# Kernel tuning notes

Measured on AMD Instinct MI355X. Metric: run time of the kernel, lower is better.

## Reference

```python
import jax, jax.numpy as jnp
import numpy as np

HIDDEN = 2048
NUM_HEADS = 32
NUM_GROUPS = 8
HEAD_DIM = HIDDEN // NUM_HEADS          # 64
GROUP_DIM = HEAD_DIM * NUM_GROUPS       # 512
HPG = NUM_HEADS // NUM_GROUPS           # heads per group = 4
B, S = 2, 2048


def setup_inputs() -> dict:
    key = jax.random.key(0)
    ks = jax.random.split(key, 6)
    sd = 1.0 / np.sqrt(HIDDEN)
    return {
        "x": jax.random.normal(ks[0], (B, S, HIDDEN), jnp.float32),
        "mask": jnp.ones((1, 1, S, S), jnp.int32),
        "Wq": jax.random.normal(ks[1], (HIDDEN, HIDDEN), jnp.float32) * sd,
        "bq": jnp.zeros((HIDDEN,), jnp.float32),
        "Wk": jax.random.normal(ks[2], (HIDDEN, GROUP_DIM), jnp.float32) * sd,
        "bk": jnp.zeros((GROUP_DIM,), jnp.float32),
        "Wv": jax.random.normal(ks[3], (HIDDEN, GROUP_DIM), jnp.float32) * sd,
        "bv": jnp.zeros((GROUP_DIM,), jnp.float32),
        "Wo": jax.random.normal(ks[4], (HIDDEN, HIDDEN), jnp.float32) * sd,
        "bo": jnp.zeros((HIDDEN,), jnp.float32),
    }


def reference(x, mask, Wq, bq, Wk, bk, Wv, bv, Wo, bo):
    b, s, _ = x.shape
    # projections
    q = x @ Wq + bq                                        # [B,S,H*d]
    k = x @ Wk + bk                                        # [B,S,G*d]
    v = x @ Wv + bv
    # split heads: q heads are group-major (g, p) to match the torch view
    q = q.reshape(b, s, NUM_GROUPS, HPG, HEAD_DIM)         # [B,S,G,P,d]
    k = k.reshape(b, s, NUM_GROUPS, HEAD_DIM)              # [B,S,G,d]
    v = v.reshape(b, s, NUM_GROUPS, HEAD_DIM)
    scale = 1.0 / np.sqrt(HEAD_DIM).astype(np.float32)
    # grouped attention without materializing repeated K/V
    scores = jnp.einsum('bsgpd,btgd->bgpst', q, k) * scale  # [B,G,P,S,T]
    if mask is not None:
        m = mask[:, :, None]                                # [1,1,1,S,T]
        scores = jnp.where(m == 0, jnp.float32(-1e9), scores)
    weights = jax.nn.softmax(scores, axis=-1)
    out = jnp.einsum('bgpst,btgd->bsgpd', weights, v)       # [B,S,G,P,d]
    out = out.reshape(b, s, HIDDEN)
    return out @ Wo + bo
```

## Files before the change

### kernel.cpp

```cpp
#include <hip/hip_runtime.h>
#include <hip/hip_bf16.h>


#define DEVINL __device__ __forceinline__

typedef __attribute__((ext_vector_type(8))) short bf16x8;
typedef __attribute__((ext_vector_type(4))) float f32x4;

DEVINL unsigned short f2bf(float f) {
  unsigned u = __builtin_bit_cast(unsigned, f);
  u += 0x7fffu + ((u >> 16) & 1u);
  return (unsigned short)(u >> 16);
}

DEVINL unsigned pk2bf(float a, float b) {
  __hip_bfloat162 h = __float22bfloat162_rn(float2{a, b});
  unsigned r;
  __builtin_memcpy(&r, &h, 4);
  return r;
}

DEVINL void gl_lds16(const void* g, void* l) {
  __builtin_amdgcn_global_load_lds(
      (const __attribute__((address_space(1))) void*)g,
      (__attribute__((address_space(3))) void*)l, 16, 0, 0);
}

__global__ __launch_bounds__(256)
void prep_k(const float* __restrict__ x,
            const float* __restrict__ Wq, const float* __restrict__ Wk,
            const float* __restrict__ Wv, const float* __restrict__ Wo,
            const int* __restrict__ mask,
            unsigned short* __restrict__ xb,
            unsigned short* __restrict__ WqT, unsigned short* __restrict__ WkT,
            unsigned short* __restrict__ WvT, unsigned short* __restrict__ WoT,
            int* __restrict__ flags)
{
  __shared__ float tile[64][68];
  __shared__ int fl[4];
  int blk = blockIdx.x;
  const int tid = threadIdx.x;
  if (blk < 4096) {
    size_t base = (size_t)blk * 2048 + tid * 8;
    float4 f0 = *(const float4*)&x[base];
    float4 f1 = *(const float4*)&x[base + 4];
    uint4 o;
    o.x = pk2bf(f0.x, f0.y); o.y = pk2bf(f0.z, f0.w);
    o.z = pk2bf(f1.x, f1.y); o.w = pk2bf(f1.z, f1.w);
    *(uint4*)&xb[base] = o;
    return;
  }
  blk -= 4096;
  if (blk >= 2560) {
    int fb = blk - 2560;
    int qt = fb >> 5, tt = fb & 31;
    bool hz = false;
#pragma unroll
    for (int it = 0; it < 8; ++it) {
      int l = it * 1024 + tid * 4;
      int row = l >> 6, col = l & 63;
      int4 mv = *(const int4*)&mask[(size_t)(qt * 128 + row) * 2048 + tt * 64 + col];
      hz |= (mv.x == 0) | (mv.y == 0) | (mv.z == 0) | (mv.w == 0);
    }
    unsigned long long bal = __ballot(hz);
    if ((tid & 63) == 0) fl[tid >> 6] = (bal != 0ull) ? 1 : 0;
    __syncthreads();
    if (tid == 0) flags[fb] = fl[0] | fl[1] | fl[2] | fl[3];
    return;
  }
  const float* W; unsigned short* WT; int N;
  if (blk < 1024)      { W = Wq; WT = WqT; N = 2048; }
  else if (blk < 1280) { W = Wk; WT = WkT; N = 512;  blk -= 1024; }
  else if (blk < 1536) { W = Wv; WT = WvT; N = 512;  blk -= 1280; }
  else                 { W = Wo; WT = WoT; N = 2048; blk -= 1536; }
  const int kt = blk & 31, nt = blk >> 5;
  const int k0 = kt * 64, n0 = nt * 64;
  const int tr = tid >> 4, tc4 = (tid & 15) * 4;
#pragma unroll
  for (int it = 0; it < 4; ++it) {
    int k = it * 16 + tr;
    float4 v = *(const float4*)&W[(size_t)(k0 + k) * N + n0 + tc4];
    tile[tc4 + 0][k] = v.x; tile[tc4 + 1][k] = v.y;
    tile[tc4 + 2][k] = v.z; tile[tc4 + 3][k] = v.w;
  }
  __syncthreads();
#pragma unroll
  for (int it = 0; it < 4; ++it) {
    int n = it * 16 + tr;
    uint2 o;
    o.x = pk2bf(tile[n][tc4 + 0], tile[n][tc4 + 1]);
    o.y = pk2bf(tile[n][tc4 + 2], tile[n][tc4 + 3]);
    *(uint2*)&WT[(size_t)(n0 + n) * 2048 + k0 + tc4] = o;
  }
}

__global__ __launch_bounds__(256)
void mm_qkv(const unsigned short* __restrict__ A,
            const unsigned short* __restrict__ Wt,
            const float* __restrict__ bq, const float* __restrict__ bk,
            const float* __restrict__ bv,
            unsigned short* __restrict__ qb, unsigned short* __restrict__ kb,
            unsigned short* __restrict__ vb)
{
  __shared__ __align__(16) unsigned short As[128 * 32];
  __shared__ __align__(16) unsigned short Bs[128 * 32];
  const int tid = threadIdx.x;
  const int lane = tid & 63, w = tid >> 6;
  const int l15 = lane & 15, quad = lane >> 4;
  const int wm = w & 1, wn = w >> 1;
  const int row0 = blockIdx.y * 128;
  const int col0 = blockIdx.x * 128;

  f32x4 acc[4][4];
#pragma unroll
  for (int mt = 0; mt < 4; ++mt)
#pragma unroll
    for (int nt = 0; nt < 4; ++nt) acc[mt][nt] = (f32x4){0.f, 0.f, 0.f, 0.f};

  const int c0 = tid, c1 = 256 + tid;
  const size_t aoff0 = (size_t)(row0 + (c0 >> 2)) * 2048 + (c0 & 3) * 8;
  const size_t aoff1 = (size_t)(row0 + (c1 >> 2)) * 2048 + (c1 & 3) * 8;
  const size_t boff0 = (size_t)(col0 + (c0 >> 2)) * 2048 + (c0 & 3) * 8;
  const size_t boff1 = (size_t)(col0 + (c1 >> 2)) * 2048 + (c1 & 3) * 8;

  for (int k0 = 0; k0 < 2048; k0 += 32) {
    gl_lds16(A + aoff0 + k0, As + (size_t)c0 * 8);
    gl_lds16(A + aoff1 + k0, As + (size_t)c1 * 8);
    gl_lds16(Wt + boff0 + k0, Bs + (size_t)c0 * 8);
    gl_lds16(Wt + boff1 + k0, Bs + (size_t)c1 * 8);
    __syncthreads();
    bf16x8 af[4], bfr[4];
#pragma unroll
    for (int mt = 0; mt < 4; ++mt)
      af[mt] = *(const bf16x8*)&As[(wm * 64 + mt * 16 + l15) * 32 + quad * 8];
#pragma unroll
    for (int nt = 0; nt < 4; ++nt)
      bfr[nt] = *(const bf16x8*)&Bs[(wn * 64 + nt * 16 + l15) * 32 + quad * 8];
#pragma unroll
    for (int mt = 0; mt < 4; ++mt)
#pragma unroll
      for (int nt = 0; nt < 4; ++nt)
        acc[mt][nt] = __builtin_amdgcn_mfma_f32_16x16x32_bf16(
            af[mt], bfr[nt], acc[mt][nt], 0, 0, 0);
    __syncthreads();
  }

  const int rbase = row0 + wm * 64 + quad * 4;
#pragma unroll
  for (int nt = 0; nt < 4; ++nt) {
    const int cg = col0 + wn * 64 + nt * 16 + l15;
#pragma unroll
    for (int mt = 0; mt < 4; ++mt) {
#pragma unroll
      for (int reg = 0; reg < 4; ++reg) {
        const int r = rbase + mt * 16 + reg;
        const int bb = r >> 11, ss = r & 2047;
        float v = acc[mt][nt][reg];
        if (col0 < 2048) {
          v += bq[cg];
          int g = cg >> 8, p = (cg >> 6) & 3, d = cg & 63;
          qb[(((size_t)((bb * 8 + g) * 4 + p)) * 2048 + ss) * 64 + d] =
              f2bf(v * 0.1803368801111244f);
        } else if (col0 < 2560) {
          int cl = cg - 2048;
          v += bk[cl];
          int g = cl >> 6, d = cl & 63;
          kb[((size_t)(bb * 8 + g) * 2048 + ss) * 64 + d] = f2bf(v);
        } else {
          int cl = cg - 2560;
          v += bv[cl];
          int g = cl >> 6, d = cl & 63;
          vb[((size_t)(bb * 8 + g) * 64 + d) * 2048 + ss] = f2bf(v);
        }
      }
    }
  }
}

__global__ __launch_bounds__(256)
void mm_out(const unsigned short* __restrict__ A,
            const unsigned short* __restrict__ Bt,
            const float* __restrict__ bias, float* __restrict__ Of)
{
  __shared__ __align__(16) unsigned short As[128 * 32];
  __shared__ __align__(16) unsigned short Bs[128 * 32];
  const int tid = threadIdx.x;
  const int lane = tid & 63, w = tid >> 6;
  const int l15 = lane & 15, quad = lane >> 4;
  const int wm = w & 1, wn = w >> 1;
  const int row0 = blockIdx.y * 128;
  const int col0 = blockIdx.x * 128;

  f32x4 acc[4][4];
#pragma unroll
  for (int mt = 0; mt < 4; ++mt)
#pragma unroll
    for (int nt = 0; nt < 4; ++nt) acc[mt][nt] = (f32x4){0.f, 0.f, 0.f, 0.f};

  const int c0 = tid, c1 = 256 + tid;
  const size_t aoff0 = (size_t)(row0 + (c0 >> 2)) * 2048 + (c0 & 3) * 8;
  const size_t aoff1 = (size_t)(row0 + (c1 >> 2)) * 2048 + (c1 & 3) * 8;
  const size_t boff0 = (size_t)(col0 + (c0 >> 2)) * 2048 + (c0 & 3) * 8;
  const size_t boff1 = (size_t)(col0 + (c1 >> 2)) * 2048 + (c1 & 3) * 8;

  for (int k0 = 0; k0 < 2048; k0 += 32) {
    gl_lds16(A + aoff0 + k0, As + (size_t)c0 * 8);
    gl_lds16(A + aoff1 + k0, As + (size_t)c1 * 8);
    gl_lds16(Bt + boff0 + k0, Bs + (size_t)c0 * 8);
    gl_lds16(Bt + boff1 + k0, Bs + (size_t)c1 * 8);
    __syncthreads();
    bf16x8 af[4], bfr[4];
#pragma unroll
    for (int mt = 0; mt < 4; ++mt)
      af[mt] = *(const bf16x8*)&As[(wm * 64 + mt * 16 + l15) * 32 + quad * 8];
#pragma unroll
    for (int nt = 0; nt < 4; ++nt)
      bfr[nt] = *(const bf16x8*)&Bs[(wn * 64 + nt * 16 + l15) * 32 + quad * 8];
#pragma unroll
    for (int mt = 0; mt < 4; ++mt)
#pragma unroll
      for (int nt = 0; nt < 4; ++nt)
        acc[mt][nt] = __builtin_amdgcn_mfma_f32_16x16x32_bf16(
            af[mt], bfr[nt], acc[mt][nt], 0, 0, 0);
    __syncthreads();
  }

  const int rbase = row0 + wm * 64 + quad * 4;
#pragma unroll
  for (int nt = 0; nt < 4; ++nt) {
    const int cg = col0 + wn * 64 + nt * 16 + l15;
    const float bvv = bias[cg];
#pragma unroll
    for (int mt = 0; mt < 4; ++mt)
#pragma unroll
      for (int reg = 0; reg < 4; ++reg) {
        const int r = rbase + mt * 16 + reg;
        Of[(size_t)r * 2048 + cg] = acc[mt][nt][reg] + bvv;
      }
  }
}

__global__ __launch_bounds__(256)
void attn_k(const unsigned short* __restrict__ qb,
            const unsigned short* __restrict__ kb,
            const unsigned short* __restrict__ vb,
            const int* __restrict__ mask, const int* __restrict__ flags,
            unsigned short* __restrict__ attnb)
{
  __shared__ __align__(16) unsigned short Ks[64 * 64];
  __shared__ __align__(16) unsigned short Vs[64 * 64];
  __shared__ __align__(16) unsigned short Ps[128 * 72];
  const int tid = threadIdx.x;
  const int lane = tid & 63, w = tid >> 6;
  const int l15 = lane & 15, quad = lane >> 4;
  const int q0 = blockIdx.x * 128;
  const int pr = blockIdx.y;
  const int b = pr >> 4, g = (pr >> 1) & 7, pp = pr & 1;
  const int bg = b * 8 + g;
  const int h0 = g * 4 + pp * 2;

  const unsigned short* Kg = kb + (size_t)bg * 2048 * 64;
  const unsigned short* Vg = vb + (size_t)bg * 64 * 2048;

  bf16x8 qf[2][2][2];
#pragma unroll
  for (int h = 0; h < 2; ++h) {
    const unsigned short* Qg = qb + (size_t)((bg * 4 + pp * 2 + h)) * 2048 * 64;
#pragma unroll
    for (int u = 0; u < 2; ++u) {
      const size_t qrow = (size_t)(q0 + w * 32 + u * 16 + l15) * 64;
      qf[h][u][0] = *(const bf16x8*)&Qg[qrow + quad * 8];
      qf[h][u][1] = *(const bf16x8*)&Qg[qrow + 32 + quad * 8];
    }
  }

  bf16x8 ones;
#pragma unroll
  for (int i = 0; i < 8; ++i) ones[i] = (short)0x3F80;

  f32x4 acc_o[2][4][2];
  f32x4 acc_l[2][2];
#pragma unroll
  for (int h = 0; h < 2; ++h) {
#pragma unroll
    for (int u = 0; u < 2; ++u) acc_l[h][u] = (f32x4){0.f, 0.f, 0.f, 0.f};
#pragma unroll
    for (int dt = 0; dt < 4; ++dt)
#pragma unroll
      for (int u = 0; u < 2; ++u) acc_o[h][dt][u] = (f32x4){0.f, 0.f, 0.f, 0.f};
  }

  const int c0 = tid, c1 = 256 + tid;
  const int kr0 = c0 >> 3, kx0 = ((c0 & 7) ^ (kr0 & 7)) * 8;
  const int kr1 = c1 >> 3, kx1 = ((c1 & 7) ^ (kr1 & 7)) * 8;

  for (int t0 = 0; t0 < 2048; t0 += 64) {
    __syncthreads();
    gl_lds16(Kg + (size_t)(t0 + kr0) * 64 + kx0, Ks + (size_t)c0 * 8);
    gl_lds16(Kg + (size_t)(t0 + kr1) * 64 + kx1, Ks + (size_t)c1 * 8);
    gl_lds16(Vg + (size_t)kr0 * 2048 + t0 + kx0, Vs + (size_t)c0 * 8);
    gl_lds16(Vg + (size_t)kr1 * 2048 + t0 + kx1, Vs + (size_t)c1 * 8);
    __syncthreads();

    bf16x8 kf[4][2];
#pragma unroll
    for (int nt = 0; nt < 4; ++nt) {
      const int trow = nt * 16 + l15, ks = trow & 7;
      kf[nt][0] = *(const bf16x8*)&Ks[trow * 64 + ((quad ^ ks) * 8)];
      kf[nt][1] = *(const bf16x8*)&Ks[trow * 64 + (((4 + quad) ^ ks) * 8)];
    }
    const bool msk = flags[blockIdx.x * 32 + (t0 >> 6)] != 0;

#pragma unroll
    for (int h = 0; h < 2; ++h) {
#pragma unroll
      for (int u = 0; u < 2; ++u) {
        f32x4 st[4];
#pragma unroll
        for (int nt = 0; nt < 4; ++nt) {
          f32x4 z = (f32x4){0.f, 0.f, 0.f, 0.f};
          z = __builtin_amdgcn_mfma_f32_16x16x32_bf16(kf[nt][0], qf[h][u][0], z, 0, 0, 0);
          st[nt] = __builtin_amdgcn_mfma_f32_16x16x32_bf16(kf[nt][1], qf[h][u][1], z, 0, 0, 0);
        }
        if (msk) {
          const size_t mrow = (size_t)(q0 + w * 32 + u * 16 + l15) * 2048;
#pragma unroll
          for (int nt = 0; nt < 4; ++nt) {
            int4 mv = *(const int4*)&mask[mrow + t0 + nt * 16 + quad * 4];
            if (mv.x == 0) st[nt][0] = -1e30f;
            if (mv.y == 0) st[nt][1] = -1e30f;
            if (mv.z == 0) st[nt][2] = -1e30f;
            if (mv.w == 0) st[nt][3] = -1e30f;
          }
        }
        const int srow = w * 32 + u * 16 + l15;
#pragma unroll
        for (int nt = 0; nt < 4; ++nt) {
          float p0 = __builtin_amdgcn_exp2f(st[nt][0]);
          float p1 = __builtin_amdgcn_exp2f(st[nt][1]);
          float p2 = __builtin_amdgcn_exp2f(st[nt][2]);
          float p3 = __builtin_amdgcn_exp2f(st[nt][3]);
          uint2 pkd;
          pkd.x = pk2bf(p0, p1);
          pkd.y = pk2bf(p2, p3);
          *(uint2*)&Ps[srow * 72 + nt * 16 + quad * 4] = pkd;
        }
      }
      asm volatile("s_waitcnt lgkmcnt(0)" ::: "memory");

      bf16x8 pf[2][2];
#pragma unroll
      for (int u = 0; u < 2; ++u) {
        const int srow = w * 32 + u * 16 + l15;
        pf[u][0] = *(const bf16x8*)&Ps[srow * 72 + quad * 8];
        pf[u][1] = *(const bf16x8*)&Ps[srow * 72 + 32 + quad * 8];
        acc_l[h][u] = __builtin_amdgcn_mfma_f32_16x16x32_bf16(ones, pf[u][0], acc_l[h][u], 0, 0, 0);
        acc_l[h][u] = __builtin_amdgcn_mfma_f32_16x16x32_bf16(ones, pf[u][1], acc_l[h][u], 0, 0, 0);
      }
#pragma unroll
      for (int dt = 0; dt < 4; ++dt) {
        const int drow = dt * 16 + l15, ks = drow & 7;
        bf16x8 v0 = *(const bf16x8*)&Vs[drow * 64 + ((quad ^ ks) * 8)];
        bf16x8 v1 = *(const bf16x8*)&Vs[drow * 64 + (((4 + quad) ^ ks) * 8)];
#pragma unroll
        for (int u = 0; u < 2; ++u) {
          acc_o[h][dt][u] = __builtin_amdgcn_mfma_f32_16x16x32_bf16(v0, pf[u][0], acc_o[h][dt][u], 0, 0, 0);
          acc_o[h][dt][u] = __builtin_amdgcn_mfma_f32_16x16x32_bf16(v1, pf[u][1], acc_o[h][dt][u], 0, 0, 0);
        }
      }
    }
  }

#pragma unroll
  for (int h = 0; h < 2; ++h) {
    const int hh = h0 + h;
#pragma unroll
    for (int u = 0; u < 2; ++u) {
      const float inv = 1.0f / acc_l[h][u][0];
      const int s = q0 + w * 32 + u * 16 + l15;
#pragma unroll
      for (int dt = 0; dt < 4; ++dt) {
        uint2 o;
        o.x = pk2bf(acc_o[h][dt][u][0] * inv, acc_o[h][dt][u][1] * inv);
        o.y = pk2bf(acc_o[h][dt][u][2] * inv, acc_o[h][dt][u][3] * inv);
        *(uint2*)&attnb[((size_t)(b * 2048 + s)) * 2048 + hh * 64 + dt * 16 + quad * 4] = o;
      }
    }
  }
}

extern "C" void kernel_launch(void* const* d_in, const int* in_sizes, int n_in,
                              void* d_out, int out_size, void* d_ws, size_t ws_size,
                              hipStream_t stream)
{
  (void)in_sizes; (void)n_in; (void)out_size; (void)ws_size;
  const float* x  = (const float*)d_in[0];
  const int* mask = (const int*)d_in[1];
  const float* Wq = (const float*)d_in[2];
  const float* bq = (const float*)d_in[3];
  const float* Wk = (const float*)d_in[4];
  const float* bk = (const float*)d_in[5];
  const float* Wv = (const float*)d_in[6];
  const float* bv = (const float*)d_in[7];
  const float* Wo = (const float*)d_in[8];
  const float* bo = (const float*)d_in[9];
  float* out = (float*)d_out;

  unsigned short* xb  = (unsigned short*)d_ws;
  unsigned short* WqT = xb  + 8388608;
  unsigned short* WkT = WqT + 4194304;
  unsigned short* WvT = WkT + 1048576;
  unsigned short* WoT = WvT + 1048576;
  unsigned short* qb  = WoT + 4194304;
  unsigned short* kb  = qb  + 8388608;
  unsigned short* vb  = kb  + 2097152;
  int* flags = (int*)(vb + 2097152);
  unsigned short* attnb = xb;

  dim3 blk(256);
  hipLaunchKernelGGL(prep_k, dim3(7168), blk, 0, stream,
                     x, Wq, Wk, Wv, Wo, mask, xb, WqT, WkT, WvT, WoT, flags);
  hipLaunchKernelGGL(mm_qkv, dim3(24, 32), blk, 0, stream,
                     xb, WqT, bq, bk, bv, qb, kb, vb);
  hipLaunchKernelGGL(attn_k, dim3(16, 32), blk, 0, stream,
                     qb, kb, vb, mask, flags, attnb);
  hipLaunchKernelGGL(mm_out, dim3(16, 32), blk, 0, stream,
                     attnb, WoT, bo, out);
}
```

Measured before the change: 354.3 us.

## Deepen GEMM K-tile with swizzled LDS and halve attention query tile

Both GEMM kernels now load 64-wide K tiles into XOR-swizzled LDS, with two MFMA half-steps per barrier pair. This halves the number of syncthreads per K and avoids LDS bank conflicts on fragment reads. The attention kernel drops from 128 to 64 query rows per block, doubling the grid, and uses a per-head P buffer with launch_bounds(256,4) for higher occupancy. The cost is more redundant K/V tile loads across attention blocks and more LDS per GEMM block.

```diff
diff --git a/kernel.cpp b/kernel.cpp
--- a/kernel.cpp
+++ b/kernel.cpp
@@ -102,14 +102,15 @@
             unsigned short* __restrict__ qb, unsigned short* __restrict__ kb,
             unsigned short* __restrict__ vb)
 {
-  __shared__ __align__(16) unsigned short As[128 * 32];
-  __shared__ __align__(16) unsigned short Bs[128 * 32];
+  __shared__ __align__(16) unsigned short As[128 * 64];
+  __shared__ __align__(16) unsigned short Bs[128 * 64];
   const int tid = threadIdx.x;
   const int lane = tid & 63, w = tid >> 6;
   const int l15 = lane & 15, quad = lane >> 4;
   const int wm = w & 1, wn = w >> 1;
   const int row0 = blockIdx.y * 128;
   const int col0 = blockIdx.x * 128;
+  const int sk = l15 & 7;
 
   f32x4 acc[4][4];
 #pragma unroll
@@ -117,31 +118,41 @@
 #pragma unroll
     for (int nt = 0; nt < 4; ++nt) acc[mt][nt] = (f32x4){0.f, 0.f, 0.f, 0.f};
 
-  const int c0 = tid, c1 = 256 + tid;
-  const size_t aoff0 = (size_t)(row0 + (c0 >> 2)) * 2048 + (c0 & 3) * 8;
-  const size_t aoff1 = (size_t)(row0 + (c1 >> 2)) * 2048 + (c1 & 3) * 8;
-  const size_t boff0 = (size_t)(col0 + (c0 >> 2)) * 2048 + (c0 & 3) * 8;
-  const size_t boff1 = (size_t)(col0 + (c1 >> 2)) * 2048 + (c1 & 3) * 8;
-
-  for (int k0 = 0; k0 < 2048; k0 += 32) {
-    gl_lds16(A + aoff0 + k0, As + (size_t)c0 * 8);
-    gl_lds16(A + aoff1 + k0, As + (size_t)c1 * 8);
-    gl_lds16(Wt + boff0 + k0, Bs + (size_t)c0 * 8);
-    gl_lds16(Wt + boff1 + k0, Bs + (size_t)c1 * 8);
-    __syncthreads();
-    bf16x8 af[4], bfr[4];
-#pragma unroll
-    for (int mt = 0; mt < 4; ++mt)
-      af[mt] = *(const bf16x8*)&As[(wm * 64 + mt * 16 + l15) * 32 + quad * 8];
-#pragma unroll
-    for (int nt = 0; nt < 4; ++nt)
-      bfr[nt] = *(const bf16x8*)&Bs[(wn * 64 + nt * 16 + l15) * 32 + quad * 8];
-#pragma unroll
-    for (int mt = 0; mt < 4; ++mt)
+  size_t aoff[4], boff[4];
+#pragma unroll
+  for (int i = 0; i < 4; ++i) {
+    const int c = tid + i * 256;
+    const int r = c >> 3, kx = ((c & 7) ^ (r & 7)) * 8;
+    aoff[i] = (size_t)(row0 + r) * 2048 + kx;
+    boff[i] = (size_t)(col0 + r) * 2048 + kx;
+  }
+
+  for (int k0 = 0; k0 < 2048; k0 += 64) {
+#pragma unroll
+    for (int i = 0; i < 4; ++i)
+      gl_lds16(A + aoff[i] + k0, As + (size_t)(tid + i * 256) * 8);
+#pragma unroll
+    for (int i = 0; i < 4; ++i)
+      gl_lds16(Wt + boff[i] + k0, Bs + (size_t)(tid + i * 256) * 8);
+    __syncthreads();
+#pragma unroll
+    for (int half = 0; half < 2; ++half) {
+      bf16x8 af[4], bfr[4];
+#pragma unroll
+      for (int mt = 0; mt < 4; ++mt)
+        af[mt] = *(const bf16x8*)&As[(wm * 64 + mt * 16 + l15) * 64 +
+                                     (((half * 4 + quad) ^ sk) * 8)];
 #pragma unroll
       for (int nt = 0; nt < 4; ++nt)
-        acc[mt][nt] = __builtin_amdgcn_mfma_f32_16x16x32_bf16(
-            af[mt], bfr[nt], acc[mt][nt], 0, 0, 0);
+        bfr[nt] = *(const bf16x8*)&Bs[(wn * 64 + nt * 16 + l15) * 64 +
+                                      (((half * 4 + quad) ^ sk) * 8)];
+#pragma unroll
+      for (int mt = 0; mt < 4; ++mt)
+#pragma unroll
+        for (int nt = 0; nt < 4; ++nt)
+          acc[mt][nt] = __builtin_amdgcn_mfma_f32_16x16x32_bf16(
+              af[mt], bfr[nt], acc[mt][nt], 0, 0, 0);
+    }
     __syncthreads();
   }
 
@@ -182,14 +193,15 @@
             const unsigned short* __restrict__ Bt,
             const float* __restrict__ bias, float* __restrict__ Of)
 {
-  __shared__ __align__(16) unsigned short As[128 * 32];
-  __shared__ __align__(16) unsigned short Bs[128 * 32];
+  __shared__ __align__(16) unsigned short As[128 * 64];
+  __shared__ __align__(16) unsigned short Bs[128 * 64];
   const int tid = threadIdx.x;
   const int lane = tid & 63, w = tid >> 6;
   const int l15 = lane & 15, quad = lane >> 4;
   const int wm = w & 1, wn = w >> 1;
   const int row0 = blockIdx.y * 128;
   const int col0 = blockIdx.x * 128;
+  const int sk = l15 & 7;
 
   f32x4 acc[4][4];
 #pragma unroll
@@ -197,31 +209,41 @@
 #pragma unroll
     for (int nt = 0; nt < 4; ++nt) acc[mt][nt] = (f32x4){0.f, 0.f, 0.f, 0.f};
 
-  const int c0 = tid, c1 = 256 + tid;
-  const size_t aoff0 = (size_t)(row0 + (c0 >> 2)) * 2048 + (c0 & 3) * 8;
-  const size_t aoff1 = (size_t)(row0 + (c1 >> 2)) * 2048 + (c1 & 3) * 8;
-  const size_t boff0 = (size_t)(col0 + (c0 >> 2)) * 2048 + (c0 & 3) * 8;
-  const size_t boff1 = (size_t)(col0 + (c1 >> 2)) * 2048 + (c1 & 3) * 8;
-
-  for (int k0 = 0; k0 < 2048; k0 += 32) {
-    gl_lds16(A + aoff0 + k0, As + (size_t)c0 * 8);
-    gl_lds16(A + aoff1 + k0, As + (size_t)c1 * 8);
-    gl_lds16(Bt + boff0 + k0, Bs + (size_t)c0 * 8);
-    gl_lds16(Bt + boff1 + k0, Bs + (size_t)c1 * 8);
-    __syncthreads();
-    bf16x8 af[4], bfr[4];
-#pragma unroll
-    for (int mt = 0; mt < 4; ++mt)
-      af[mt] = *(const bf16x8*)&As[(wm * 64 + mt * 16 + l15) * 32 + quad * 8];
-#pragma unroll
-    for (int nt = 0; nt < 4; ++nt)
-      bfr[nt] = *(const bf16x8*)&Bs[(wn * 64 + nt * 16 + l15) * 32 + quad * 8];
-#pragma unroll
-    for (int mt = 0; mt < 4; ++mt)
+  size_t aoff[4], boff[4];
+#pragma unroll
+  for (int i = 0; i < 4; ++i) {
+    const int c = tid + i * 256;
+    const int r = c >> 3, kx = ((c & 7) ^ (r & 7)) * 8;
+    aoff[i] = (size_t)(row0 + r) * 2048 + kx;
+    boff[i] = (size_t)(col0 + r) * 2048 + kx;
+  }
+
+  for (int k0 = 0; k0 < 2048; k0 += 64) {
+#pragma unroll
+    for (int i = 0; i < 4; ++i)
+      gl_lds16(A + aoff[i] + k0, As + (size_t)(tid + i * 256) * 8);
+#pragma unroll
+    for (int i = 0; i < 4; ++i)
+      gl_lds16(Bt + boff[i] + k0, Bs + (size_t)(tid + i * 256) * 8);
+    __syncthreads();
+#pragma unroll
+    for (int half = 0; half < 2; ++half) {
+      bf16x8 af[4], bfr[4];
+#pragma unroll
+      for (int mt = 0; mt < 4; ++mt)
+        af[mt] = *(const bf16x8*)&As[(wm * 64 + mt * 16 + l15) * 64 +
+                                     (((half * 4 + quad) ^ sk) * 8)];
 #pragma unroll
       for (int nt = 0; nt < 4; ++nt)
-        acc[mt][nt] = __builtin_amdgcn_mfma_f32_16x16x32_bf16(
-            af[mt], bfr[nt], acc[mt][nt], 0, 0, 0);
+        bfr[nt] = *(const bf16x8*)&Bs[(wn * 64 + nt * 16 + l15) * 64 +
+                                      (((half * 4 + quad) ^ sk) * 8)];
+#pragma unroll
+      for (int mt = 0; mt < 4; ++mt)
+#pragma unroll
+        for (int nt = 0; nt < 4; ++nt)
+          acc[mt][nt] = __builtin_amdgcn_mfma_f32_16x16x32_bf16(
+              af[mt], bfr[nt], acc[mt][nt], 0, 0, 0);
+    }
     __syncthreads();
   }
 
@@ -240,7 +262,7 @@
   }
 }
 
-__global__ __launch_bounds__(256)
+__global__ __launch_bounds__(256, 4)
 void attn_k(const unsigned short* __restrict__ qb,
             const unsigned short* __restrict__ kb,
             const unsigned short* __restrict__ vb,
@@ -249,11 +271,11 @@
 {
   __shared__ __align__(16) unsigned short Ks[64 * 64];
   __shared__ __align__(16) unsigned short Vs[64 * 64];
-  __shared__ __align__(16) unsigned short Ps[128 * 72];
+  __shared__ __align__(16) unsigned short Ps[2][64 * 72];
   const int tid = threadIdx.x;
   const int lane = tid & 63, w = tid >> 6;
   const int l15 = lane & 15, quad = lane >> 4;
-  const int q0 = blockIdx.x * 128;
+  const int q0 = blockIdx.x * 64;
   const int pr = blockIdx.y;
   const int b = pr >> 4, g = (pr >> 1) & 7, pp = pr & 1;
   const int bg = b * 8 + g;
@@ -262,37 +284,33 @@
   const unsigned short* Kg = kb + (size_t)bg * 2048 * 64;
   const unsigned short* Vg = vb + (size_t)bg * 64 * 2048;
 
-  bf16x8 qf[2][2][2];
+  bf16x8 qf[2][2];
 #pragma unroll
   for (int h = 0; h < 2; ++h) {
-    const unsigned short* Qg = qb + (size_t)((bg * 4 + pp * 2 + h)) * 2048 * 64;
-#pragma unroll
-    for (int u = 0; u < 2; ++u) {
-      const size_t qrow = (size_t)(q0 + w * 32 + u * 16 + l15) * 64;
-      qf[h][u][0] = *(const bf16x8*)&Qg[qrow + quad * 8];
-      qf[h][u][1] = *(const bf16x8*)&Qg[qrow + 32 + quad * 8];
-    }
+    const unsigned short* Qg = qb + (size_t)(bg * 4 + pp * 2 + h) * 2048 * 64;
+    const size_t qrow = (size_t)(q0 + w * 16 + l15) * 64;
+    qf[h][0] = *(const bf16x8*)&Qg[qrow + quad * 8];
+    qf[h][1] = *(const bf16x8*)&Qg[qrow + 32 + quad * 8];
   }
 
   bf16x8 ones;
 #pragma unroll
   for (int i = 0; i < 8; ++i) ones[i] = (short)0x3F80;
 
-  f32x4 acc_o[2][4][2];
-  f32x4 acc_l[2][2];
+  f32x4 acc_o[2][4];
+  f32x4 acc_l[2];
 #pragma unroll
   for (int h = 0; h < 2; ++h) {
-#pragma unroll
-    for (int u = 0; u < 2; ++u) acc_l[h][u] = (f32x4){0.f, 0.f, 0.f, 0.f};
-#pragma unroll
-    for (int dt = 0; dt < 4; ++dt)
-#pragma unroll
-      for (int u = 0; u < 2; ++u) acc_o[h][dt][u] = (f32x4){0.f, 0.f, 0.f, 0.f};
+    acc_l[h] = (f32x4){0.f, 0.f, 0.f, 0.f};
+#pragma unroll
+    for (int dt = 0; dt < 4; ++dt) acc_o[h][dt] = (f32x4){0.f, 0.f, 0.f, 0.f};
   }
 
   const int c0 = tid, c1 = 256 + tid;
   const int kr0 = c0 >> 3, kx0 = ((c0 & 7) ^ (kr0 & 7)) * 8;
   const int kr1 = c1 >> 3, kx1 = ((c1 & 7) ^ (kr1 & 7)) * 8;
+  const int sk = l15 & 7;
+  const int srow = w * 16 + l15;
 
   for (int t0 = 0; t0 < 2048; t0 += 64) {
     __syncthreads();
@@ -305,68 +323,59 @@
     bf16x8 kf[4][2];
 #pragma unroll
     for (int nt = 0; nt < 4; ++nt) {
-      const int trow = nt * 16 + l15, ks = trow & 7;
-      kf[nt][0] = *(const bf16x8*)&Ks[trow * 64 + ((quad ^ ks) * 8)];
-      kf[nt][1] = *(const bf16x8*)&Ks[trow * 64 + (((4 + quad) ^ ks) * 8)];
-    }
-    const bool msk = flags[blockIdx.x * 32 + (t0 >> 6)] != 0;
+      const int trow = nt * 16 + l15;
+      kf[nt][0] = *(const bf16x8*)&Ks[trow * 64 + ((quad ^ sk) * 8)];
+      kf[nt][1] = *(const bf16x8*)&Ks[trow * 64 + (((4 + quad) ^ sk) * 8)];
+    }
+    const bool msk = flags[(blockIdx.x >> 1) * 32 + (t0 >> 6)] != 0;
 
 #pragma unroll
     for (int h = 0; h < 2; ++h) {
-#pragma unroll
-      for (int u = 0; u < 2; ++u) {
-        f32x4 st[4];
+      f32x4 st[4];
+#pragma unroll
+      for (int nt = 0; nt < 4; ++nt) {
+        f32x4 z = (f32x4){0.f, 0.f, 0.f, 0.f};
+        z = __builtin_amdgcn_mfma_f32_16x16x32_bf16(kf[nt][0], qf[h][0], z, 0, 0, 0);
+        st[nt] = __builtin_amdgcn_mfma_f32_16x16x32_bf16(kf[nt][1], qf[h][1], st[nt] = z, 0, 0, 0);
+      }
+      if (msk) {
+        const size_t mrow = (size_t)(q0 + srow) * 2048;
 #pragma unroll
         for (int nt = 0; nt < 4; ++nt) {
-          f32x4 z = (f32x4){0.f, 0.f, 0.f, 0.f};
-          z = __builtin_amdgcn_mfma_f32_16x16x32_bf16(kf[nt][0], qf[h][u][0], z, 0, 0, 0);
-          st[nt] = __builtin_amdgcn_mfma_f32_16x16x32_bf16(kf[nt][1], qf[h][u][1], z, 0, 0, 0);
+          int4 mv = *(const int4*)&mask[mrow + t0 + nt * 16 + quad * 4];
+          if (mv.x == 0) st[nt][0] = -1e30f;
+          if (mv.y == 0) st[nt][1] = -1e30f;
+          if (mv.z == 0) st[nt][2] = -1e30f;
+          if (mv.w == 0) st[nt][3] = -1e30f;
         }
-        if (msk) {
-          const size_t mrow = (size_t)(q0 + w * 32 + u * 16 + l15) * 2048;
-#pragma unroll
-          for (int nt = 0; nt < 4; ++nt) {
-            int4 mv = *(const int4*)&mask[mrow + t0 + nt * 16 + quad * 4];
-            if (mv.x == 0) st[nt][0] = -1e30f;
-            if (mv.y == 0) st[nt][1] = -1e30f;
-            if (mv.z == 0) st[nt][2] = -1e30f;
-            if (mv.w == 0) st[nt][3] = -1e30f;
-          }
-        }
-        const int srow = w * 32 + u * 16 + l15;
-#pragma unroll
-        for (int nt = 0; nt < 4; ++nt) {
-          float p0 = __builtin_amdgcn_exp2f(st[nt][0]);
-          float p1 = __builtin_amdgcn_exp2f(st[nt][1]);
-          float p2 = __builtin_amdgcn_exp2f(st[nt][2]);
-          float p3 = __builtin_amdgcn_exp2f(st[nt][3]);
-          uint2 pkd;
-          pkd.x = pk2bf(p0, p1);
-          pkd.y = pk2bf(p2, p3);
-          *(uint2*)&Ps[srow * 72 + nt * 16 + quad * 4] = pkd;
-        }
-      }
-      asm volatile("s_waitcnt lgkmcnt(0)" ::: "memory");
-
-      bf16x8 pf[2][2];
-#pragma unroll
-      for (int u = 0; u < 2; ++u) {
-        const int srow = w * 32 + u * 16 + l15;
-        pf[u][0] = *(const bf16x8*)&Ps[srow * 72 + quad * 8];
-        pf[u][1] = *(const bf16x8*)&Ps[srow * 72 + 32 + quad * 8];
-        acc_l[h][u] = __builtin_amdgcn_mfma_f32_16x16x32_bf16(ones, pf[u][0], acc_l[h][u], 0, 0, 0);
-        acc_l[h][u] = __builtin_amdgcn_mfma_f32_16x16x32_bf16(ones, pf[u][1], acc_l[h][u], 0, 0, 0);
-      }
+      }
+#pragma unroll
+      for (int nt = 0; nt < 4; ++nt) {
+        float p0 = __builtin_amdgcn_exp2f(st[nt][0]);
+        float p1 = __builtin_amdgcn_exp2f(st[nt][1]);
+        float p2 = __builtin_amdgcn_exp2f(st[nt][2]);
+        float p3 = __builtin_amdgcn_exp2f(st[nt][3]);
+        uint2 pkd;
+        pkd.x = pk2bf(p0, p1);
+        pkd.y = pk2bf(p2, p3);
+        *(uint2*)&Ps[h][srow * 72 + nt * 16 + quad * 4] = pkd;
+      }
+    }
+    asm volatile("s_waitcnt lgkmcnt(0)" ::: "memory");
+
+#pragma unroll
+    for (int h = 0; h < 2; ++h) {
+      bf16x8 pf0 = *(const bf16x8*)&Ps[h][srow * 72 + quad * 8];
+      bf16x8 pf1 = *(const bf16x8*)&Ps[h][srow * 72 + 32 + quad * 8];
+      acc_l[h] = __builtin_amdgcn_mfma_f32_16x16x32_bf16(ones, pf0, acc_l[h], 0, 0, 0);
+      acc_l[h] = __builtin_amdgcn_mfma_f32_16x16x32_bf16(ones, pf1, acc_l[h], 0, 0, 0);
 #pragma unroll
       for (int dt = 0; dt < 4; ++dt) {
-        const int drow = dt * 16 + l15, ks = drow & 7;
-        bf16x8 v0 = *(const bf16x8*)&Vs[drow * 64 + ((quad ^ ks) * 8)];
-        bf16x8 v1 = *(const bf16x8*)&Vs[drow * 64 + (((4 + quad) ^ ks) * 8)];
-#pragma unroll
-        for (int u = 0; u < 2; ++u) {
-          acc_o[h][dt][u] = __builtin_amdgcn_mfma_f32_16x16x32_bf16(v0, pf[u][0], acc_o[h][dt][u], 0, 0, 0);
-          acc_o[h][dt][u] = __builtin_amdgcn_mfma_f32_16x16x32_bf16(v1, pf[u][1], acc_o[h][dt][u], 0, 0, 0);
-        }
+        const int drow = dt * 16 + l15;
+        bf16x8 v0 = *(const bf16x8*)&Vs[drow * 64 + ((quad ^ sk) * 8)];
+        bf16x8 v1 = *(const bf16x8*)&Vs[drow * 64 + (((4 + quad) ^ sk) * 8)];
+        acc_o[h][dt] = __builtin_amdgcn_mfma_f32_16x16x32_bf16(v0, pf0, acc_o[h][dt], 0, 0, 0);
+        acc_o[h][dt] = __builtin_amdgcn_mfma_f32_16x16x32_bf16(v1, pf1, acc_o[h][dt], 0, 0, 0);
       }
     }
   }
@@ -374,17 +383,14 @@
 #pragma unroll
   for (int h = 0; h < 2; ++h) {
     const int hh = h0 + h;
-#pragma unroll
-    for (int u = 0; u < 2; ++u) {
-      const float inv = 1.0f / acc_l[h][u][0];
-      const int s = q0 + w * 32 + u * 16 + l15;
-#pragma unroll
-      for (int dt = 0; dt < 4; ++dt) {
-        uint2 o;
-        o.x = pk2bf(acc_o[h][dt][u][0] * inv, acc_o[h][dt][u][1] * inv);
-        o.y = pk2bf(acc_o[h][dt][u][2] * inv, acc_o[h][dt][u][3] * inv);
-        *(uint2*)&attnb[((size_t)(b * 2048 + s)) * 2048 + hh * 64 + dt * 16 + quad * 4] = o;
-      }
+    const float inv = 1.0f / acc_l[h][0];
+    const int s = q0 + srow;
+#pragma unroll
+    for (int dt = 0; dt < 4; ++dt) {
+      uint2 o;
+      o.x = pk2bf(acc_o[h][dt][0] * inv, acc_o[h][dt][1] * inv);
+      o.y = pk2bf(acc_o[h][dt][2] * inv, acc_o[h][dt][3] * inv);
+      *(uint2*)&attnb[((size_t)(b * 2048 + s)) * 2048 + hh * 64 + dt * 16 + quad * 4] = o;
     }
   }
 }
@@ -422,7 +428,7 @@
                      x, Wq, Wk, Wv, Wo, mask, xb, WqT, WkT, WvT, WoT, flags);
   hipLaunchKernelGGL(mm_qkv, dim3(24, 32), blk, 0, stream,
                      xb, WqT, bq, bk, bv, qb, kb, vb);
-  hipLaunchKernelGGL(attn_k, dim3(16, 32), blk, 0, stream,
+  hipLaunchKernelGGL(attn_k, dim3(32, 32), blk, 0, stream,
                      qb, kb, vb, mask, flags, attnb);
   hipLaunchKernelGGL(mm_out, dim3(16, 32), blk, 0, stream,
                      attnb, WoT, bo, out);
```

Result: slower. 363.5 us (+2.6%).
